# Kernel tuning notes

Measured on AMD Instinct MI355X. Metric: run time of the kernel, lower is better.

The kernel has to match this reference:

```python
import jax, jax.numpy as jnp
import numpy as np

N = 100000   # nodes
E = 1600000  # edges (avg degree 16)
D = 64       # in_dim == hidden_dim
L = 3        # num_layers
EPS = 1e-5   # LayerNorm eps


def setup_inputs() -> dict:
    key = jax.random.key(0)
    k0, k1, k2 = jax.random.split(key, 3)
    x = jax.random.normal(k0, (N, D), dtype=jnp.float32)
    edge_index = jax.random.randint(k1, (2, E), 0, N, dtype=jnp.int32)
    # Per-layer GCN weights/bias (Glorot-ish scale) and LayerNorm params
    Ws = jax.random.normal(k2, (L, D, D), dtype=jnp.float32) / np.float32(np.sqrt(D))
    bs = jnp.zeros((L, D), dtype=jnp.float32)
    gammas = jnp.ones((L, D), dtype=jnp.float32)
    betas = jnp.zeros((L, D), dtype=jnp.float32)
    return {"x": x, "Ws": Ws, "bs": bs, "gammas": gammas, "betas": betas,
            "edge_index": edge_index}


def _layer_norm(h, gamma, beta):
    mu = jnp.mean(h, axis=-1, keepdims=True)
    var = jnp.mean(jnp.square(h - mu), axis=-1, keepdims=True)
    return (h - mu) * jax.lax.rsqrt(var + EPS) * gamma + beta


def reference(x, Ws, bs, gammas, betas, edge_index):
    # GCNConv semantics: add self-loops, symmetric deg^{-1/2} normalization.
    loop = jnp.arange(N, dtype=edge_index.dtype)
    row = jnp.concatenate([edge_index[0], loop])  # source (gather)
    col = jnp.concatenate([edge_index[1], loop])  # target (scatter)
    deg = jax.ops.segment_sum(jnp.ones_like(col, dtype=x.dtype), col, num_segments=N)
    dinv = jnp.where(deg > 0, jax.lax.rsqrt(deg), jnp.zeros_like(deg))
    enorm = dinv[row] * dinv[col]  # (E+N,)

    h = x
    for i in range(L):
        hw = h @ Ws[i]                                   # (N, D) small GEMM
        msg = hw[row] * enorm[:, None]                   # (E+N, D) gather
        h = jax.ops.segment_sum(msg, col, num_segments=N) + bs[i]  # scatter-add
        h = _layer_norm(h, gammas[i], betas[i])
        if i < L - 1:
            h = jax.nn.relu(h)                           # dropout is identity in eval
    return h
```

## Files before the change

kernel.cpp:

```cpp
#include <hip/hip_runtime.h>
#include <hip/hip_bf16.h>


#define DDIM 64
#define EPSV 1e-5f
#define BSHIFT 9
#define BNODES (1 << BSHIFT)
#define NBUCK 256
#define CHUNK 4096
#define CBLKS 256

typedef __hip_bfloat16 bf16;
typedef unsigned int u32;
typedef unsigned short u16;
typedef unsigned long long u64;
typedef __attribute__((ext_vector_type(8))) short frag8;
typedef __attribute__((ext_vector_type(4))) float f32x4;

__device__ __forceinline__ float b2f(bf16 v) { return __bfloat162float(v); }
__device__ __forceinline__ float lo2f(u32 u) {
    union { u32 x; float f; } c; c.x = u << 16; return c.f;
}
__device__ __forceinline__ float hi2f(u32 u) {
    union { u32 x; float f; } c; c.x = u & 0xffff0000u; return c.f;
}
__device__ __forceinline__ u32 packbf(float a, float b) {
    union { bf16 h; u16 u; } ca, cb;
    ca.h = __float2bfloat16(a);
    cb.h = __float2bfloat16(b);
    return (u32)ca.u | ((u32)cb.u << 16);
}
__device__ __forceinline__ float cvt_load(const void* src, int i, int f32) {
    return f32 ? ((const float*)src)[i] : b2f(((const bf16*)src)[i]);
}


__global__ void __launch_bounds__(256) bucket_count(const int* __restrict__ col,
                                                    int* __restrict__ partials,
                                                    const u32* __restrict__ g,
                                                    int* __restrict__ flagF32, int E) {
    __shared__ int h[NBUCK];
    int tid = threadIdx.x;
    if (blockIdx.x == 0 && tid == 0) *flagF32 = (g[0] == 0x3F800000u) ? 1 : 0;
    h[tid] = 0;
    __syncthreads();
    for (int i = blockIdx.x * blockDim.x + tid; i < E; i += gridDim.x * blockDim.x)
        atomicAdd(&h[col[i] >> BSHIFT], 1);
    __syncthreads();
    partials[blockIdx.x * NBUCK + tid] = h[tid];
}

__global__ void bucket_scan(const int* __restrict__ partials, int* __restrict__ bbase,
                            int* __restrict__ gcur, int nbuck, int E) {
    __shared__ int s[NBUCK];
    int tid = threadIdx.x;
    int v = 0;
    for (int b = 0; b < CBLKS; b++) v += partials[b * NBUCK + tid];
    s[tid] = v;
    __syncthreads();
    for (int off = 1; off < NBUCK; off <<= 1) {
        int t = (tid >= off) ? s[tid - off] : 0;
        __syncthreads();
        s[tid] += t;
        __syncthreads();
    }
    int excl = s[tid] - v;
    if (tid < nbuck) { bbase[tid] = excl; gcur[tid] = excl; }
    if (tid == 0) bbase[nbuck] = E;
}

__global__ void __launch_bounds__(256) partition_edges(const int* __restrict__ row,
                                                       const int* __restrict__ col,
                                                       int* __restrict__ gcur,
                                                       u64* __restrict__ pairs, int E) {
    __shared__ int hist[NBUCK];
    __shared__ int lbase[NBUCK];
    __shared__ int gdelta[NBUCK];
    __shared__ int lcur[NBUCK];
    __shared__ int sbuf[NBUCK];
    __shared__ int dest[CHUNK];
    __shared__ u64 stage[CHUNK];
    int tid = threadIdx.x;
    int chunk0 = blockIdx.x * CHUNK;
    hist[tid] = 0;
    lcur[tid] = 0;
    __syncthreads();
    int r[16], c[16];
#pragma unroll
    for (int i = 0; i < 16; i++) {
        int idx = chunk0 + i * 256 + tid;
        if (idx < E) {
            r[i] = row[idx];
            c[i] = col[idx];
            atomicAdd(&hist[c[i] >> BSHIFT], 1);
        }
    }
    __syncthreads();
    int h = hist[tid];
    sbuf[tid] = h;
    __syncthreads();
    for (int off = 1; off < 256; off <<= 1) {
        int t = (tid >= off) ? sbuf[tid - off] : 0;
        __syncthreads();
        sbuf[tid] += t;
        __syncthreads();
    }
    int excl = sbuf[tid] - h;
    lbase[tid] = excl;
    int gb = (h > 0) ? atomicAdd(&gcur[tid], h) : 0;
    gdelta[tid] = gb - excl;
    __syncthreads();
#pragma unroll
    for (int i = 0; i < 16; i++) {
        int idx = chunk0 + i * 256 + tid;
        if (idx < E) {
            int b = c[i] >> BSHIFT;
            int pos = lbase[b] + atomicAdd(&lcur[b], 1);
            stage[pos] = ((u64)(u32)c[i] << 32) | (u32)r[i];
            dest[pos] = gdelta[b];
        }
    }
    __syncthreads();
    int chunkN = min(CHUNK, E - chunk0);
    for (int j = tid; j < chunkN; j += 256)
        pairs[(size_t)(dest[j] + j)] = stage[j];
}

__global__ void __launch_bounds__(512) build_csr(const u64* __restrict__ pairs,
                                                 const int* __restrict__ bbase,
                                                 int* __restrict__ ptr,
                                                 int* __restrict__ srcs,
                                                 float* __restrict__ dinv,
                                                 const void* __restrict__ W,
                                                 const void* __restrict__ bsv,
                                                 const void* __restrict__ gsv,
                                                 const void* __restrict__ btv,
                                                 bf16* __restrict__ dWt,
                                                 bf16* __restrict__ db,
                                                 bf16* __restrict__ dg,
                                                 bf16* __restrict__ dbt,
                                                 const int* __restrict__ flagF32,
                                                 int nbuck, int N, int E) {
    __shared__ int deg[BNODES];
    __shared__ int lptr[BNODES];
    __shared__ int lfill[BNODES];
    int b = blockIdx.x;
    int tid = threadIdx.x;
    if (b >= nbuck) {
        int f = *flagF32;
        for (int i = tid; i < 3 * 4096; i += 512) {
            int L = i >> 12, n = (i >> 6) & 63, k = i & 63;
            dWt[i] = __float2bfloat16(cvt_load(W, (L << 12) | (k << 6) | n, f));
        }
        for (int i = tid; i < 192; i += 512) {
            db[i]  = __float2bfloat16(cvt_load(bsv, i, f));
            dg[i]  = __float2bfloat16(cvt_load(gsv, i, f));
            dbt[i] = __float2bfloat16(cvt_load(btv, i, f));
        }
        return;
    }
    int node0 = b << BSHIFT;
    int nn = min(BNODES, N - node0);
    deg[tid] = 0;
    lfill[tid] = 0;
    __syncthreads();
    int beg = bbase[b], end = bbase[b + 1];
    for (int i = beg + tid; i < end; i += 512)
        atomicAdd(&deg[(int)(pairs[i] >> 32) - node0], 1);
    __syncthreads();
    int d = deg[tid];
    lptr[tid] = d;
    __syncthreads();
    for (int off = 1; off < BNODES; off <<= 1) {
        int t = (tid >= off) ? lptr[tid - off] : 0;
        __syncthreads();
        lptr[tid] += t;
        __syncthreads();
    }
    int excl = lptr[tid] - d;
    lptr[tid] = beg + excl;
    if (tid < nn) {
        ptr[node0 + tid] = beg + excl;
        dinv[node0 + tid] = rsqrtf((float)(d + 1));
    }
    if (b == 0 && tid == 0) ptr[N] = E;
    __syncthreads();
    for (int i = beg + tid; i < end; i += 512) {
        u64 pr = pairs[i];
        int li = (int)(pr >> 32) - node0;
        int p = lptr[li] + atomicAdd(&lfill[li], 1);
        srcs[p] = (int)(pr & 0xffffffffu);
    }
}

__global__ void __launch_bounds__(256) convert_h(const void* __restrict__ x,
                                                 const float* __restrict__ dinv,
                                                 bf16* __restrict__ H,
                                                 const int* __restrict__ flagF32,
                                                 int nX8) {
    int i = blockIdx.x * 256 + threadIdx.x;
    if (i >= nX8) return;
    int f = *flagF32;
    float dv = dinv[i >> 3];
    uint4 out;
    if (f) {
        const float4* p = (const float4*)((const float*)x + (size_t)i * 8);
        float4 u = p[0], v = p[1];
        out.x = packbf(u.x * dv, u.y * dv);
        out.y = packbf(u.z * dv, u.w * dv);
        out.z = packbf(v.x * dv, v.y * dv);
        out.w = packbf(v.z * dv, v.w * dv);
    } else {
        uint4 u = *(const uint4*)((const bf16*)x + (size_t)i * 8);
        out.x = packbf(lo2f(u.x) * dv, hi2f(u.x) * dv);
        out.y = packbf(lo2f(u.y) * dv, hi2f(u.y) * dv);
        out.z = packbf(lo2f(u.z) * dv, hi2f(u.z) * dv);
        out.w = packbf(lo2f(u.w) * dv, hi2f(u.w) * dv);
    }
    ((uint4*)H)[i] = out;
}


#define LOADG(g) \
    if (m > (g) * 8) { \
        int s0 = __shfl(sidx, bl + (g) * 8 + sub, 64); \
        int s1 = __shfl(sidx, bl + (g) * 8 + 4 + sub, 64); \
        qa##g = ((const uint4*)(Hs + ((size_t)s0 << 6)))[quad]; \
        qb##g = ((const uint4*)(Hs + ((size_t)s1 << 6)))[quad]; \
    }

#define FMAG(g) \
    if (m > (g) * 8) { \
        float k0 = ((g) * 8 + sub < m) ? 1.f : 0.f; \
        float k1 = ((g) * 8 + 4 + sub < m) ? 1.f : 0.f; \
        a0 = fmaf(lo2f(qa##g.x), k0, a0); a1 = fmaf(hi2f(qa##g.x), k0, a1); \
        a2 = fmaf(lo2f(qa##g.y), k0, a2); a3 = fmaf(hi2f(qa##g.y), k0, a3); \
        a4 = fmaf(lo2f(qa##g.z), k0, a4); a5 = fmaf(hi2f(qa##g.z), k0, a5); \
        a6 = fmaf(lo2f(qa##g.w), k0, a6); a7 = fmaf(hi2f(qa##g.w), k0, a7); \
        a0 = fmaf(lo2f(qb##g.x), k1, a0); a1 = fmaf(hi2f(qb##g.x), k1, a1); \
        a2 = fmaf(lo2f(qb##g.y), k1, a2); a3 = fmaf(hi2f(qb##g.y), k1, a3); \
        a4 = fmaf(lo2f(qb##g.z), k1, a4); a5 = fmaf(hi2f(qb##g.z), k1, a5); \
        a6 = fmaf(lo2f(qb##g.w), k1, a6); a7 = fmaf(hi2f(qb##g.w), k1, a7); \
    }

__global__ void __launch_bounds__(256, 4) fused_layer(const bf16* __restrict__ Hs,
                                                      const int* __restrict__ ptr,
                                                      const int* __restrict__ srcs,
                                                      const float* __restrict__ dinv,
                                                      const bf16* __restrict__ Wt,
                                                      const bf16* __restrict__ bias,
                                                      const bf16* __restrict__ gamma,
                                                      const bf16* __restrict__ beta,
                                                      bf16* __restrict__ outB,
                                                      float* __restrict__ outF,
                                                      const int* __restrict__ flagF32,
                                                      const float* __restrict__ dscale,
                                                      int relu, int last, int N) {
    __shared__ __align__(16) bf16 lsA[4][16][64];
    int tid = threadIdx.x;
    int wv = tid >> 6, lane = tid & 63;
    int half = lane >> 5, lane32 = lane & 31;
    int sub = lane32 >> 3, quad = lane & 7;
    int r0 = blockIdx.x * 64 + wv * 16;

    int myrow = r0 + (lane & 15);
    int mb = 0, me = 0;
    float mdv = 0.f;
    if (myrow < N) {
        mb = ptr[myrow];
        me = ptr[myrow + 1];
        mdv = dinv[myrow];
    }

    int sid0[8];
#pragma unroll
    for (int it = 0; it < 8; it++) {
        int rl = it * 2 + half;
        int pb = __shfl(mb, rl, 64);
        int dd = __shfl(me, rl, 64) - pb;
        int s = 0;
        if (lane32 < dd) s = srcs[pb + lane32];
        sid0[it] = s;
    }

#pragma unroll
    for (int it = 0; it < 8; it++) {
        int rl = it * 2 + half;
        int v = r0 + rl;
        int vc = v < N ? v : N - 1;
        uint4 selfq = ((const uint4*)(Hs + ((size_t)vc << 6)))[quad];
        int beg = __shfl(mb, rl, 64);
        int end = __shfl(me, rl, 64);
        int m = end - beg;
        if (m > 32) m = 32;
        int sidx = sid0[it];
        int bl = half << 5;
        uint4 qa0, qb0, qa1, qb1, qa2, qb2, qa3, qb3;
        LOADG(0)
        LOADG(1)
        LOADG(2)
        LOADG(3)
        float a0 = 0.f, a1 = 0.f, a2 = 0.f, a3 = 0.f;
        float a4 = 0.f, a5 = 0.f, a6 = 0.f, a7 = 0.f;
        FMAG(0)
        FMAG(1)
        FMAG(2)
        FMAG(3)
        for (int base = beg + 32; base < end; base += 32) {
            int rem = end - base;
            int m2 = rem < 32 ? rem : 32;
            int sx = 0;
            if (lane32 < m2) sx = srcs[base + lane32];
            for (int j = 0; j < m2; j += 8) {
                int e0 = j + sub;
                int e1 = j + 4 + sub;
                int s0 = __shfl(sx, bl + e0, 64);
                int s1 = __shfl(sx, bl + e1, 64);
                float k0 = (e0 < m2) ? 1.f : 0.f;
                float k1 = (e1 < m2) ? 1.f : 0.f;
                uint4 q0 = ((const uint4*)(Hs + ((size_t)s0 << 6)))[quad];
                uint4 q1 = ((const uint4*)(Hs + ((size_t)s1 << 6)))[quad];
                a0 = fmaf(lo2f(q0.x), k0, a0); a1 = fmaf(hi2f(q0.x), k0, a1);
                a2 = fmaf(lo2f(q0.y), k0, a2); a3 = fmaf(hi2f(q0.y), k0, a3);
                a4 = fmaf(lo2f(q0.z), k0, a4); a5 = fmaf(hi2f(q0.z), k0, a5);
                a6 = fmaf(lo2f(q0.w), k0, a6); a7 = fmaf(hi2f(q0.w), k0, a7);
                a0 = fmaf(lo2f(q1.x), k1, a0); a1 = fmaf(hi2f(q1.x), k1, a1);
                a2 = fmaf(lo2f(q1.y), k1, a2); a3 = fmaf(hi2f(q1.y), k1, a3);
                a4 = fmaf(lo2f(q1.z), k1, a4); a5 = fmaf(hi2f(q1.z), k1, a5);
                a6 = fmaf(lo2f(q1.w), k1, a6); a7 = fmaf(hi2f(q1.w), k1, a7);
            }
        }
#pragma unroll
        for (int d = 8; d < 32; d <<= 1) {
            a0 += __shfl_xor(a0, d, 64); a1 += __shfl_xor(a1, d, 64);
            a2 += __shfl_xor(a2, d, 64); a3 += __shfl_xor(a3, d, 64);
            a4 += __shfl_xor(a4, d, 64); a5 += __shfl_xor(a5, d, 64);
            a6 += __shfl_xor(a6, d, 64); a7 += __shfl_xor(a7, d, 64);
        }
        float dv = __shfl(mdv, rl, 64);
        if (sub == 0 && v < N) {
            a0 += lo2f(selfq.x); a1 += hi2f(selfq.x);
            a2 += lo2f(selfq.y); a3 += hi2f(selfq.y);
            a4 += lo2f(selfq.z); a5 += hi2f(selfq.z);
            a6 += lo2f(selfq.w); a7 += hi2f(selfq.w);
            uint4 o;
            o.x = packbf(a0 * dv, a1 * dv);
            o.y = packbf(a2 * dv, a3 * dv);
            o.z = packbf(a4 * dv, a5 * dv);
            o.w = packbf(a6 * dv, a7 * dv);
            *(uint4*)&lsA[wv][rl][quad * 8] = o;
        }
    }

    int n = lane & 15, q = lane >> 4;
    frag8 af0 = *(const frag8*)&lsA[wv][n][q * 8];
    frag8 af1 = *(const frag8*)&lsA[wv][n][32 + q * 8];

    f32x4 acc[4];
#pragma unroll
    for (int t = 0; t < 4; t++) acc[t] = (f32x4){0.f, 0.f, 0.f, 0.f};
#pragma unroll
    for (int t = 0; t < 4; t++) {
        const uint4* bp = (const uint4*)(Wt + (((size_t)(t * 16 + n)) << 6));
        frag8 bf0 = __builtin_bit_cast(frag8, bp[q]);
        frag8 bf1 = __builtin_bit_cast(frag8, bp[4 + q]);
        acc[t] = __builtin_amdgcn_mfma_f32_16x16x32_bf16(af0, bf0, acc[t], 0, 0, 0);
        acc[t] = __builtin_amdgcn_mfma_f32_16x16x32_bf16(af1, bf1, acc[t], 0, 0, 0);
    }

    float bb[4], gg[4], be[4];
#pragma unroll
    for (int t = 0; t < 4; t++) {
        int c = t * 16 + n;
        bb[t] = b2f(bias[c]);
        gg[t] = b2f(gamma[c]);
        be[t] = b2f(beta[c]);
    }
    int f32o = last ? flagF32[0] : 0;

#pragma unroll
    for (int r = 0; r < 4; r++) {
        int rr = r0 + q * 4 + r;
        float v0 = acc[0][r] + bb[0];
        float v1 = acc[1][r] + bb[1];
        float v2 = acc[2][r] + bb[2];
        float v3 = acc[3][r] + bb[3];
        float s = v0 + v1 + v2 + v3;
        s += __shfl_xor(s, 1, 64);
        s += __shfl_xor(s, 2, 64);
        s += __shfl_xor(s, 4, 64);
        s += __shfl_xor(s, 8, 64);
        float mu = s * (1.f / 64.f);
        float d0 = v0 - mu, d1 = v1 - mu, d2 = v2 - mu, d3 = v3 - mu;
        float sq = d0 * d0 + d1 * d1 + d2 * d2 + d3 * d3;
        sq += __shfl_xor(sq, 1, 64);
        sq += __shfl_xor(sq, 2, 64);
        sq += __shfl_xor(sq, 4, 64);
        sq += __shfl_xor(sq, 8, 64);
        float rs = rsqrtf(sq * (1.f / 64.f) + EPSV);
        float o0 = d0 * rs * gg[0] + be[0];
        float o1 = d1 * rs * gg[1] + be[1];
        float o2 = d2 * rs * gg[2] + be[2];
        float o3 = d3 * rs * gg[3] + be[3];
        if (relu) {
            o0 = fmaxf(o0, 0.f); o1 = fmaxf(o1, 0.f);
            o2 = fmaxf(o2, 0.f); o3 = fmaxf(o3, 0.f);
        }
        if (rr < N) {
            if (dscale) {
                float sc = dscale[rr];
                o0 *= sc; o1 *= sc; o2 *= sc; o3 *= sc;
            }
            size_t base = ((size_t)rr << 6) + n;
            if (f32o) {
                outF[base] = o0; outF[base + 16] = o1;
                outF[base + 32] = o2; outF[base + 48] = o3;
            } else {
                outB[base] = __float2bfloat16(o0);
                outB[base + 16] = __float2bfloat16(o1);
                outB[base + 32] = __float2bfloat16(o2);
                outB[base + 48] = __float2bfloat16(o3);
            }
        }
    }
}


extern "C" void kernel_launch(void* const* d_in, const int* in_sizes, int n_in,
                              void* d_out, int out_size, void* d_ws, size_t ws_size,
                              hipStream_t stream) {
    (void)n_in; (void)out_size; (void)ws_size;
    const void* x      = d_in[0];
    const void* Wsrc   = d_in[1];
    const void* bsrc   = d_in[2];
    const void* gsrc   = d_in[3];
    const void* btsrc  = d_in[4];
    const int*  ei     = (const int*)d_in[5];
    int N = in_sizes[0] / DDIM;
    int E = in_sizes[5] / 2;
    const int* rowp = ei;
    const int* colp = ei + E;

    char* w = (char*)d_ws;
    auto alloc = [&](size_t bytes) -> char* {
        char* p = w;
        w += (bytes + 255) / 256 * 256;
        return p;
    };
    int*   flag  = (int*)alloc(4);
    int*   gcur  = (int*)alloc(NBUCK * 4);
    int*   parts = (int*)alloc((size_t)CBLKS * NBUCK * 4);
    int*   bbase = (int*)alloc((NBUCK + 1) * 4);
    int*   ptr   = (int*)alloc((size_t)(N + 1) * 4);
    int*   srcs  = (int*)alloc((size_t)E * 4);
    float* dinv  = (float*)alloc((size_t)N * 4);
    bf16*  H     = (bf16*)alloc((size_t)N * DDIM * 2);
    u64*   pairs = (u64*)alloc((size_t)E * 8);
    bf16*  wsW   = (bf16*)alloc((size_t)3 * 4096 * 2);
    bf16*  wsB   = (bf16*)alloc(192 * 2);
    bf16*  wsG   = (bf16*)alloc(192 * 2);
    bf16*  wsBt  = (bf16*)alloc(192 * 2);
    bf16*  H2    = (bf16*)alloc((size_t)N * DDIM * 2);

    const int tb = 256;
    int nbuck = (N + BNODES - 1) >> BSHIFT;
    bucket_count<<<CBLKS, tb, 0, stream>>>(colp, parts, (const u32*)gsrc, flag, E);
    bucket_scan<<<1, NBUCK, 0, stream>>>(parts, bbase, gcur, nbuck, E);
    partition_edges<<<(E + CHUNK - 1) / CHUNK, tb, 0, stream>>>(rowp, colp, gcur, pairs, E);
    build_csr<<<nbuck + 1, 512, 0, stream>>>(pairs, bbase, ptr, srcs, dinv,
                                             Wsrc, bsrc, gsrc, btsrc,
                                             wsW, wsB, wsG, wsBt,
                                             flag, nbuck, N, E);

    int nX8 = N * DDIM / 8;
    convert_h<<<(nX8 + tb - 1) / tb, tb, 0, stream>>>(x, dinv, H, flag, nX8);

    int gBlocks = (N + 63) / 64;
    fused_layer<<<gBlocks, tb, 0, stream>>>(H, ptr, srcs, dinv,
                                            wsW + 0 * 4096, wsB + 0,   wsG + 0,   wsBt + 0,
                                            H2, nullptr, flag, dinv, 1, 0, N);
    fused_layer<<<gBlocks, tb, 0, stream>>>(H2, ptr, srcs, dinv,
                                            wsW + 1 * 4096, wsB + 64,  wsG + 64,  wsBt + 64,
                                            H, nullptr, flag, dinv, 1, 0, N);
    fused_layer<<<gBlocks, tb, 0, stream>>>(H, ptr, srcs, dinv,
                                            wsW + 2 * 4096, wsB + 128, wsG + 128, wsBt + 128,
                                            (bf16*)d_out, (float*)d_out, flag, nullptr, 0, 1, N);
}
```

Before: 253.8 us.

## Double-buffer neighbor gathers in fused layer and use finer edge buckets

The per-row aggregation loop in fused_layer becomes a software pipeline with two register sets (A/B), so the gathers for the next row pair are issued before the FMAs for the current pair. This is meant to hide gather latency behind the accumulation. Separately, CSR construction switches to 256-node buckets (512 buckets) and partition_edges now runs with 512 threads, so build_csr gets more blocks with less work each. The pipelining roughly doubles live vector registers, which could cut occupancy under the 256,4 launch bounds.

```diff
diff --git a/kernel.cpp b/kernel.cpp
--- a/kernel.cpp
+++ b/kernel.cpp
@@ -4,9 +4,9 @@
 
 #define DDIM 64
 #define EPSV 1e-5f
-#define BSHIFT 9
+#define BSHIFT 8
 #define BNODES (1 << BSHIFT)
-#define NBUCK 256
+#define NBUCK 512
 #define CHUNK 4096
 #define CBLKS 256
 
@@ -43,11 +43,13 @@
     int tid = threadIdx.x;
     if (blockIdx.x == 0 && tid == 0) *flagF32 = (g[0] == 0x3F800000u) ? 1 : 0;
     h[tid] = 0;
+    h[tid + 256] = 0;
     __syncthreads();
     for (int i = blockIdx.x * blockDim.x + tid; i < E; i += gridDim.x * blockDim.x)
         atomicAdd(&h[col[i] >> BSHIFT], 1);
     __syncthreads();
     partials[blockIdx.x * NBUCK + tid] = h[tid];
+    partials[blockIdx.x * NBUCK + tid + 256] = h[tid + 256];
 }
 
 __global__ void bucket_scan(const int* __restrict__ partials, int* __restrict__ bbase,
@@ -69,7 +71,7 @@
     if (tid == 0) bbase[nbuck] = E;
 }
 
-__global__ void __launch_bounds__(256) partition_edges(const int* __restrict__ row,
+__global__ void __launch_bounds__(512) partition_edges(const int* __restrict__ row,
                                                        const int* __restrict__ col,
                                                        int* __restrict__ gcur,
                                                        u64* __restrict__ pairs, int E) {
@@ -85,10 +87,10 @@
     hist[tid] = 0;
     lcur[tid] = 0;
     __syncthreads();
-    int r[16], c[16];
-#pragma unroll
-    for (int i = 0; i < 16; i++) {
-        int idx = chunk0 + i * 256 + tid;
+    int r[CHUNK / 512], c[CHUNK / 512];
+#pragma unroll
+    for (int i = 0; i < CHUNK / 512; i++) {
+        int idx = chunk0 + i * 512 + tid;
         if (idx < E) {
             r[i] = row[idx];
             c[i] = col[idx];
@@ -99,7 +101,7 @@
     int h = hist[tid];
     sbuf[tid] = h;
     __syncthreads();
-    for (int off = 1; off < 256; off <<= 1) {
+    for (int off = 1; off < NBUCK; off <<= 1) {
         int t = (tid >= off) ? sbuf[tid - off] : 0;
         __syncthreads();
         sbuf[tid] += t;
@@ -111,8 +113,8 @@
     gdelta[tid] = gb - excl;
     __syncthreads();
 #pragma unroll
-    for (int i = 0; i < 16; i++) {
-        int idx = chunk0 + i * 256 + tid;
+    for (int i = 0; i < CHUNK / 512; i++) {
+        int idx = chunk0 + i * 512 + tid;
         if (idx < E) {
             int b = c[i] >> BSHIFT;
             int pos = lbase[b] + atomicAdd(&lcur[b], 1);
@@ -122,7 +124,7 @@
     }
     __syncthreads();
     int chunkN = min(CHUNK, E - chunk0);
-    for (int j = tid; j < chunkN; j += 256)
+    for (int j = tid; j < chunkN; j += 512)
         pairs[(size_t)(dest[j] + j)] = stage[j];
 }
 
@@ -161,24 +163,23 @@
     }
     int node0 = b << BSHIFT;
     int nn = min(BNODES, N - node0);
-    deg[tid] = 0;
-    lfill[tid] = 0;
+    if (tid < BNODES) { deg[tid] = 0; lfill[tid] = 0; }
     __syncthreads();
     int beg = bbase[b], end = bbase[b + 1];
     for (int i = beg + tid; i < end; i += 512)
         atomicAdd(&deg[(int)(pairs[i] >> 32) - node0], 1);
     __syncthreads();
-    int d = deg[tid];
-    lptr[tid] = d;
+    int d = (tid < BNODES) ? deg[tid] : 0;
+    if (tid < BNODES) lptr[tid] = d;
     __syncthreads();
     for (int off = 1; off < BNODES; off <<= 1) {
-        int t = (tid >= off) ? lptr[tid - off] : 0;
+        int t = (tid >= off && tid < BNODES) ? lptr[tid - off] : 0;
         __syncthreads();
-        lptr[tid] += t;
+        if (tid < BNODES) lptr[tid] += t;
         __syncthreads();
     }
-    int excl = lptr[tid] - d;
-    lptr[tid] = beg + excl;
+    int excl = (tid < BNODES) ? lptr[tid] - d : 0;
+    if (tid < BNODES) lptr[tid] = beg + excl;
     if (tid < nn) {
         ptr[node0 + tid] = beg + excl;
         dinv[node0 + tid] = rsqrtf((float)(d + 1));
@@ -221,26 +222,101 @@
 }
 
 
-#define LOADG(g) \
-    if (m > (g) * 8) { \
-        int s0 = __shfl(sidx, bl + (g) * 8 + sub, 64); \
-        int s1 = __shfl(sidx, bl + (g) * 8 + 4 + sub, 64); \
-        qa##g = ((const uint4*)(Hs + ((size_t)s0 << 6)))[quad]; \
-        qb##g = ((const uint4*)(Hs + ((size_t)s1 << 6)))[quad]; \
-    }
-
-#define FMAG(g) \
-    if (m > (g) * 8) { \
-        float k0 = ((g) * 8 + sub < m) ? 1.f : 0.f; \
-        float k1 = ((g) * 8 + 4 + sub < m) ? 1.f : 0.f; \
-        a0 = fmaf(lo2f(qa##g.x), k0, a0); a1 = fmaf(hi2f(qa##g.x), k0, a1); \
-        a2 = fmaf(lo2f(qa##g.y), k0, a2); a3 = fmaf(hi2f(qa##g.y), k0, a3); \
-        a4 = fmaf(lo2f(qa##g.z), k0, a4); a5 = fmaf(hi2f(qa##g.z), k0, a5); \
-        a6 = fmaf(lo2f(qa##g.w), k0, a6); a7 = fmaf(hi2f(qa##g.w), k0, a7); \
-        a0 = fmaf(lo2f(qb##g.x), k1, a0); a1 = fmaf(hi2f(qb##g.x), k1, a1); \
-        a2 = fmaf(lo2f(qb##g.y), k1, a2); a3 = fmaf(hi2f(qb##g.y), k1, a3); \
-        a4 = fmaf(lo2f(qb##g.z), k1, a4); a5 = fmaf(hi2f(qb##g.z), k1, a5); \
-        a6 = fmaf(lo2f(qb##g.w), k1, a6); a7 = fmaf(hi2f(qb##g.w), k1, a7); \
+#define LG(S, g, sx_) \
+    { \
+        int s0_ = __shfl(sx_, bl + (g) * 8 + sub, 64); \
+        int s1_ = __shfl(sx_, bl + (g) * 8 + 4 + sub, 64); \
+        qa##g##S = ((const uint4*)(Hs + ((size_t)s0_ << 6)))[quad]; \
+        qb##g##S = ((const uint4*)(Hs + ((size_t)s1_ << 6)))[quad]; \
+    }
+
+#define LOADSET(S, IT) \
+    { \
+        int rl_ = (IT) * 2 + half; \
+        int v_ = r0 + rl_; \
+        int vc_ = v_ < N ? v_ : N - 1; \
+        self##S = ((const uint4*)(Hs + ((size_t)vc_ << 6)))[quad]; \
+        int beg_ = __shfl(mb, rl_, 64); \
+        int end_ = __shfl(me, rl_, 64); \
+        beg##S = beg_; \
+        end##S = end_; \
+        int m_ = end_ - beg_; \
+        m##S = m_ > 32 ? 32 : m_; \
+        int sx_ = sid0[IT]; \
+        if (m##S > 0)  LG(S, 0, sx_) \
+        if (m##S > 8)  LG(S, 1, sx_) \
+        if (m##S > 16) LG(S, 2, sx_) \
+        if (m##S > 24) LG(S, 3, sx_) \
+    }
+
+#define FG(S, g) \
+    if (m##S > (g) * 8) { \
+        float k0 = ((g) * 8 + sub < m##S) ? 1.f : 0.f; \
+        float k1 = ((g) * 8 + 4 + sub < m##S) ? 1.f : 0.f; \
+        a0 = fmaf(lo2f(qa##g##S.x), k0, a0); a1 = fmaf(hi2f(qa##g##S.x), k0, a1); \
+        a2 = fmaf(lo2f(qa##g##S.y), k0, a2); a3 = fmaf(hi2f(qa##g##S.y), k0, a3); \
+        a4 = fmaf(lo2f(qa##g##S.z), k0, a4); a5 = fmaf(hi2f(qa##g##S.z), k0, a5); \
+        a6 = fmaf(lo2f(qa##g##S.w), k0, a6); a7 = fmaf(hi2f(qa##g##S.w), k0, a7); \
+        a0 = fmaf(lo2f(qb##g##S.x), k1, a0); a1 = fmaf(hi2f(qb##g##S.x), k1, a1); \
+        a2 = fmaf(lo2f(qb##g##S.y), k1, a2); a3 = fmaf(hi2f(qb##g##S.y), k1, a3); \
+        a4 = fmaf(lo2f(qb##g##S.z), k1, a4); a5 = fmaf(hi2f(qb##g##S.z), k1, a5); \
+        a6 = fmaf(lo2f(qb##g##S.w), k1, a6); a7 = fmaf(hi2f(qb##g##S.w), k1, a7); \
+    }
+
+#define FMASET(S, IT) \
+    { \
+        int rl_ = (IT) * 2 + half; \
+        int v_ = r0 + rl_; \
+        float a0 = 0.f, a1 = 0.f, a2 = 0.f, a3 = 0.f; \
+        float a4 = 0.f, a5 = 0.f, a6 = 0.f, a7 = 0.f; \
+        FG(S, 0) \
+        FG(S, 1) \
+        FG(S, 2) \
+        FG(S, 3) \
+        for (int base = beg##S + 32; base < end##S; base += 32) {  \
+            int rem = end##S - base; \
+            int m2 = rem < 32 ? rem : 32; \
+            int sx = 0; \
+            if (lane32 < m2) sx = srcs[base + lane32]; \
+            for (int j = 0; j < m2; j += 8) { \
+                int e0 = j + sub; \
+                int e1 = j + 4 + sub; \
+                int s0 = __shfl(sx, bl + e0, 64); \
+                int s1 = __shfl(sx, bl + e1, 64); \
+                float k0 = (e0 < m2) ? 1.f : 0.f; \
+                float k1 = (e1 < m2) ? 1.f : 0.f; \
+                uint4 q0 = ((const uint4*)(Hs + ((size_t)s0 << 6)))[quad]; \
+                uint4 q1 = ((const uint4*)(Hs + ((size_t)s1 << 6)))[quad]; \
+                a0 = fmaf(lo2f(q0.x), k0, a0); a1 = fmaf(hi2f(q0.x), k0, a1); \
+                a2 = fmaf(lo2f(q0.y), k0, a2); a3 = fmaf(hi2f(q0.y), k0, a3); \
+                a4 = fmaf(lo2f(q0.z), k0, a4); a5 = fmaf(hi2f(q0.z), k0, a5); \
+                a6 = fmaf(lo2f(q0.w), k0, a6); a7 = fmaf(hi2f(q0.w), k0, a7); \
+                a0 = fmaf(lo2f(q1.x), k1, a0); a1 = fmaf(hi2f(q1.x), k1, a1); \
+                a2 = fmaf(lo2f(q1.y), k1, a2); a3 = fmaf(hi2f(q1.y), k1, a3); \
+                a4 = fmaf(lo2f(q1.z), k1, a4); a5 = fmaf(hi2f(q1.z), k1, a5); \
+                a6 = fmaf(lo2f(q1.w), k1, a6); a7 = fmaf(hi2f(q1.w), k1, a7); \
+            } \
+        } \
+        _Pragma("unroll") \
+        for (int dd = 8; dd < 32; dd <<= 1) { \
+            a0 += __shfl_xor(a0, dd, 64); a1 += __shfl_xor(a1, dd, 64); \
+            a2 += __shfl_xor(a2, dd, 64); a3 += __shfl_xor(a3, dd, 64); \
+            a4 += __shfl_xor(a4, dd, 64); a5 += __shfl_xor(a5, dd, 64); \
+            a6 += __shfl_xor(a6, dd, 64); a7 += __shfl_xor(a7, dd, 64); \
+        } \
+        float dv = __shfl(mdv, rl_, 64); \
+        if (sub == 0 && v_ < N) { \
+            a0 += lo2f(self##S.x); a1 += hi2f(self##S.x); \
+            a2 += lo2f(self##S.y); a3 += hi2f(self##S.y); \
+            a4 += lo2f(self##S.z); a5 += hi2f(self##S.z); \
+            a6 += lo2f(self##S.w); a7 += hi2f(self##S.w); \
+            uint4 o; \
+            o.x = packbf(a0 * dv, a1 * dv); \
+            o.y = packbf(a2 * dv, a3 * dv); \
+            o.z = packbf(a4 * dv, a5 * dv); \
+            o.w = packbf(a6 * dv, a7 * dv); \
+            *(uint4*)&lsA[wv][rl_][quad * 8] = o; \
+        } \
     }
 
 __global__ void __launch_bounds__(256, 4) fused_layer(const bf16* __restrict__ Hs,
@@ -261,6 +337,7 @@
     int wv = tid >> 6, lane = tid & 63;
     int half = lane >> 5, lane32 = lane & 31;
     int sub = lane32 >> 3, quad = lane & 7;
+    int bl = half << 5;
     int r0 = blockIdx.x * 64 + wv * 16;
 
     int myrow = r0 + (lane & 15);
@@ -283,74 +360,19 @@
         sid0[it] = s;
     }
 
-#pragma unroll
-    for (int it = 0; it < 8; it++) {
-        int rl = it * 2 + half;
-        int v = r0 + rl;
-        int vc = v < N ? v : N - 1;
-        uint4 selfq = ((const uint4*)(Hs + ((size_t)vc << 6)))[quad];
-        int beg = __shfl(mb, rl, 64);
-        int end = __shfl(me, rl, 64);
-        int m = end - beg;
-        if (m > 32) m = 32;
-        int sidx = sid0[it];
-        int bl = half << 5;
-        uint4 qa0, qb0, qa1, qb1, qa2, qb2, qa3, qb3;
-        LOADG(0)
-        LOADG(1)
-        LOADG(2)
-        LOADG(3)
-        float a0 = 0.f, a1 = 0.f, a2 = 0.f, a3 = 0.f;
-        float a4 = 0.f, a5 = 0.f, a6 = 0.f, a7 = 0.f;
-        FMAG(0)
-        FMAG(1)
-        FMAG(2)
-        FMAG(3)
-        for (int base = beg + 32; base < end; base += 32) {
-            int rem = end - base;
-            int m2 = rem < 32 ? rem : 32;
-            int sx = 0;
-            if (lane32 < m2) sx = srcs[base + lane32];
-            for (int j = 0; j < m2; j += 8) {
-                int e0 = j + sub;
-                int e1 = j + 4 + sub;
-                int s0 = __shfl(sx, bl + e0, 64);
-                int s1 = __shfl(sx, bl + e1, 64);
-                float k0 = (e0 < m2) ? 1.f : 0.f;
-                float k1 = (e1 < m2) ? 1.f : 0.f;
-                uint4 q0 = ((const uint4*)(Hs + ((size_t)s0 << 6)))[quad];
-                uint4 q1 = ((const uint4*)(Hs + ((size_t)s1 << 6)))[quad];
-                a0 = fmaf(lo2f(q0.x), k0, a0); a1 = fmaf(hi2f(q0.x), k0, a1);
-                a2 = fmaf(lo2f(q0.y), k0, a2); a3 = fmaf(hi2f(q0.y), k0, a3);
-                a4 = fmaf(lo2f(q0.z), k0, a4); a5 = fmaf(hi2f(q0.z), k0, a5);
-                a6 = fmaf(lo2f(q0.w), k0, a6); a7 = fmaf(hi2f(q0.w), k0, a7);
-                a0 = fmaf(lo2f(q1.x), k1, a0); a1 = fmaf(hi2f(q1.x), k1, a1);
-                a2 = fmaf(lo2f(q1.y), k1, a2); a3 = fmaf(hi2f(q1.y), k1, a3);
-                a4 = fmaf(lo2f(q1.z), k1, a4); a5 = fmaf(hi2f(q1.z), k1, a5);
-                a6 = fmaf(lo2f(q1.w), k1, a6); a7 = fmaf(hi2f(q1.w), k1, a7);
-            }
-        }
-#pragma unroll
-        for (int d = 8; d < 32; d <<= 1) {
-            a0 += __shfl_xor(a0, d, 64); a1 += __shfl_xor(a1, d, 64);
-            a2 += __shfl_xor(a2, d, 64); a3 += __shfl_xor(a3, d, 64);
-            a4 += __shfl_xor(a4, d, 64); a5 += __shfl_xor(a5, d, 64);
-            a6 += __shfl_xor(a6, d, 64); a7 += __shfl_xor(a7, d, 64);
-        }
-        float dv = __shfl(mdv, rl, 64);
-        if (sub == 0 && v < N) {
-            a0 += lo2f(selfq.x); a1 += hi2f(selfq.x);
-            a2 += lo2f(selfq.y); a3 += hi2f(selfq.y);
-            a4 += lo2f(selfq.z); a5 += hi2f(selfq.z);
-            a6 += lo2f(selfq.w); a7 += hi2f(selfq.w);
-            uint4 o;
-            o.x = packbf(a0 * dv, a1 * dv);
-            o.y = packbf(a2 * dv, a3 * dv);
-            o.z = packbf(a4 * dv, a5 * dv);
-            o.w = packbf(a6 * dv, a7 * dv);
-            *(uint4*)&lsA[wv][rl][quad * 8] = o;
-        }
-    }
+    uint4 qa0A, qa1A, qa2A, qa3A, qb0A, qb1A, qb2A, qb3A, selfA;
+    uint4 qa0B, qa1B, qa2B, qa3B, qb0B, qb1B, qb2B, qb3B, selfB;
+    int mA, begA, endA, mB, begB, endB;
+
+    LOADSET(A, 0)
+    LOADSET(B, 1) FMASET(A, 0)
+    LOADSET(A, 2) FMASET(B, 1)
+    LOADSET(B, 3) FMASET(A, 2)
+    LOADSET(A, 4) FMASET(B, 3)
+    LOADSET(B, 5) FMASET(A, 4)
+    LOADSET(A, 6) FMASET(B, 5)
+    LOADSET(B, 7) FMASET(A, 6)
+    FMASET(B, 7)
 
     int n = lane & 15, q = lane >> 4;
     frag8 af0 = *(const frag8*)&lsA[wv][n][q * 8];
@@ -466,7 +488,7 @@
     int nbuck = (N + BNODES - 1) >> BSHIFT;
     bucket_count<<<CBLKS, tb, 0, stream>>>(colp, parts, (const u32*)gsrc, flag, E);
     bucket_scan<<<1, NBUCK, 0, stream>>>(parts, bbase, gcur, nbuck, E);
-    partition_edges<<<(E + CHUNK - 1) / CHUNK, tb, 0, stream>>>(rowp, colp, gcur, pairs, E);
+    partition_edges<<<(E + CHUNK - 1) / CHUNK, 512, 0, stream>>>(rowp, colp, gcur, pairs, E);
     build_csr<<<nbuck + 1, 512, 0, stream>>>(pairs, bbase, ptr, srcs, dinv,
                                              Wsrc, bsrc, gsrc, btsrc,
                                              wsW, wsB, wsG, wsBt,
```

Result: slower. 263.0 us (+3.6%).
